# Kernel tuning notes

Measured on AMD Instinct MI355X. Metric: run time of the kernel, lower is better.

## Reference

```python
import jax, jax.numpy as jnp
import numpy as np

RATIO = 0.5          # drop_config[0]; gradually=False so epoch scaling is unused
NUM_BATCHES = 32     # number of distinct batch indices in the sparse coords


def setup_inputs() -> dict:
    key = jax.random.key(0)
    k1, k2, k3 = jax.random.split(key, 3)
    N, C = 1_000_000, 64
    batch_idx = jnp.sort(jax.random.randint(k1, (N,), 0, NUM_BATCHES)).astype(jnp.int32)
    feats = jax.random.normal(k2, (N, C), dtype=jnp.float32)
    scores = jax.random.uniform(k3, (N,), dtype=jnp.float32)  # per-point sampling key
    return {"feats": feats, "batch_idx": batch_idx, "scores": scores}


def _keep_mask(batch_idx, scores):
    """Per batch segment b, drop the floor(n_b * RATIO) points with lowest score
    (equivalent in distribution to np.random.choice without replacement)."""
    N = scores.shape[0]
    counts = jax.ops.segment_sum(jnp.ones((N,), jnp.int32), batch_idx,
                                 num_segments=NUM_BATCHES)              # [B]
    starts = jnp.cumsum(counts) - counts                                 # exclusive prefix [B]
    order = jnp.lexsort((scores, batch_idx))                             # sort by (batch, score)
    pos = jnp.zeros((N,), jnp.int32).at[order].set(
        jnp.arange(N, dtype=jnp.int32))                                  # global sorted position
    rank = pos - starts[batch_idx]                                       # rank within own segment
    n_drop = jnp.floor(counts.astype(jnp.float32) * RATIO).astype(jnp.int32)
    return (rank >= n_drop[batch_idx]).astype(scores.dtype)              # 1 = keep, 0 = dropped


def reference(feats, batch_idx, scores):
    # MinkowskiPruning removes dropped rows; with static shapes we express the
    # identical math as masking features to zero (the module's alternate return path).
    mask = _keep_mask(batch_idx, scores)
    return feats * mask[:, None]
```

## Files before the change

### kernel.cpp

```cpp
#include <hip/hip_runtime.h>
#include <stdint.h>

#define NBATCH 32
#define NSUB   64
#define SUBCAP 128
#define CAPTOT 6144
#define CAP2   512

typedef unsigned long long u64;
typedef unsigned int u32;
typedef float f4 __attribute__((ext_vector_type(4)));

struct WsHdr {
  u64 keysel[NBATCH];
  int counts[NBATCH];
};

__device__ __forceinline__ u32 ordbits(float s) {
  u32 u = __float_as_uint(s);
  return (u & 0x80000000u) ? ~u : (u | 0x80000000u);
}
__device__ __forceinline__ u32 obL() { return ordbits(0.46f); }
__device__ __forceinline__ u32 obR() { return ordbits(0.54f); }


__global__ void k_zero(u32* __restrict__ p, int nwords) {
  int stride = gridDim.x * blockDim.x;
  for (int i = blockIdx.x * blockDim.x + threadIdx.x; i < nwords; i += stride)
    p[i] = 0u;
}

__global__ void k_pass1(const int* __restrict__ batch, const float* __restrict__ scores,
                        int n, u32* __restrict__ meta, u64* __restrict__ cand) {
  __shared__ int h[NBATCH], hl[NBATCH];
  if (threadIdx.x < NBATCH) { h[threadIdx.x] = 0; hl[threadIdx.x] = 0; }
  __syncthreads();
  int sub = blockIdx.x & (NSUB - 1);
  int i = blockIdx.x * blockDim.x + threadIdx.x;
  if (i < n) {
    int b = batch[i];
    u32 ob = ordbits(scores[i]);
    bool lo = ob < obL();
    u64 act = __ballot(1);
    int lead = (int)__ffsll((long long)act) - 1;
    int b0 = __shfl(b, lead, 64);
    bool uni = (__ballot(b == b0) == act);
    if (uni) {
      u64 lom = __ballot(lo);
      if ((threadIdx.x & 63) == lead) {
        atomicAdd(&h[b0], (int)__popcll(act));
        if (lom) atomicAdd(&hl[b0], (int)__popcll(lom));
      }
    } else {
      atomicAdd(&h[b], 1);
      if (lo) atomicAdd(&hl[b], 1);
    }
    if (!lo && ob < obR()) {
      int cell = (b << 6) | sub;
      int p = (int)atomicAdd(&meta[(cell << 4) + 2], 1u);
      if (p < SUBCAP)
        cand[(size_t)cell * SUBCAP + p] = ((u64)ob << 24) | (u32)i;
    }
  }
  __syncthreads();
  if (threadIdx.x < NBATCH) {
    int cell = (threadIdx.x << 6) | sub;
    if (h[threadIdx.x])  atomicAdd(&meta[(cell << 4) + 0], (u32)h[threadIdx.x]);
    if (hl[threadIdx.x]) atomicAdd(&meta[(cell << 4) + 1], (u32)hl[threadIdx.x]);
  }
}

__global__ void k_final(const float* __restrict__ scores, const u32* __restrict__ meta,
                        const u64* __restrict__ cand, WsHdr* ws) {
  __shared__ u64 ck[CAPTOT];
  __shared__ u64 ck2[CAP2];
  __shared__ int sc[256];
  __shared__ int moff[NSUB + 1];
  __shared__ int sh_w, sh_krem, sh_m2, sh_cnt, sh_clo, sh_bad, sh_start;
  int b = blockIdx.x, t = threadIdx.x;

  if (t < NSUB) {
    const u32* mp = meta + (((b << 6) | t) << 4);
    int mc = (int)mp[0], ml = (int)mp[1], mw = (int)mp[2];
    u64 bad = __ballot(mw > SUBCAP);
    int v = mw < SUBCAP ? mw : SUBCAP;
    for (int d = 1; d < 64; d <<= 1) { int u = __shfl_up(v, d, 64); if (t >= d) v += u; }
    moff[t + 1] = v; if (t == 0) moff[0] = 0;
    int s1 = mc, s2 = ml;
    for (int off = 32; off > 0; off >>= 1) {
      s1 += __shfl_down(s1, off, 64);
      s2 += __shfl_down(s2, off, 64);
    }
    if (t == 0) { sh_cnt = s1; sh_clo = s2; sh_bad = (bad != 0ull); }
  }
  __syncthreads();
  int cnt = sh_cnt;
  if (cnt == 0) { if (t == 0) ws->keysel[b] = 0ull; return; }
  int krem = cnt >> 1;
  int m = moff[NSUB];
  int krem2 = krem - sh_clo;
  bool fast = !sh_bad && krem2 >= 0 && krem2 < m && m <= CAPTOT;

  if (fast) {
    const u32 span = obR() - obL();
    for (int sub = 0; sub < NSUB; ++sub) {
      int cw = moff[sub + 1] - moff[sub];
      const u64* src = cand + (size_t)((b << 6) | sub) * SUBCAP;
      for (int j = t; j < cw; j += 256) ck[moff[sub] + j] = src[j];
    }
    sc[t] = 0;
    if (t == 0) sh_m2 = 0;
    __syncthreads();
    for (int j = t; j < m; j += 256) {
      u32 ob = (u32)(ck[j] >> 24);
      u32 bk = (u32)(((u64)(ob - obL()) << 8) / span);
      atomicAdd(&sc[bk], 1);
    }
    __syncthreads();
    int own = sc[t];
    for (int off = 1; off < 256; off <<= 1) {
      int v = (t >= off) ? sc[t - off] : 0;
      __syncthreads(); sc[t] += v; __syncthreads();
    }
    int excl = sc[t] - own;
    if (krem2 >= excl && krem2 < excl + own) { sh_w = t; sh_krem = krem2 - excl; }
    __syncthreads();
    int W = sh_w, krem3 = sh_krem;
    for (int j = t; j < m; j += 256) {
      u32 ob = (u32)(ck[j] >> 24);
      u32 bk = (u32)(((u64)(ob - obL()) << 8) / span);
      if ((int)bk == W) {
        int p = atomicAdd(&sh_m2, 1);
        if (p < CAP2) ck2[p] = ck[j];
      }
    }
    __syncthreads();
    int m2 = sh_m2;
    if (m2 <= CAP2) {
      for (int j = t; j < m2; j += 256) {
        u64 key = ck2[j];
        int r = 0;
        for (int q = 0; q < m2; ++q) r += (ck2[q] < key);
        if (r == krem3) ws->keysel[b] = key;
      }
      return;
    }
    __syncthreads();
  }

  {
    int acc = 0;
    for (int idx = t; idx < b * NSUB; idx += 256)
      acc += (int)meta[((idx / NSUB) == (idx / NSUB) ? (((idx / NSUB) << 6) | (idx & (NSUB - 1))) : 0) << 4];
    sc[t] = acc; __syncthreads();
    for (int off = 128; off > 0; off >>= 1) {
      if (t < off) sc[t] += sc[t + off];
      __syncthreads();
    }
    if (t == 0) sh_start = sc[0];
    __syncthreads();
  }
  int start = sh_start;
  u64 prefix = 0; int kr = krem;
  for (int shift = 48; shift >= 0; shift -= 8) {
    sc[t] = 0;
    __syncthreads();
    for (int idx = t; idx < cnt; idx += 256) {
      u64 key = ((u64)ordbits(scores[start + idx]) << 24) | (u32)(start + idx);
      if ((key >> (shift + 8)) == prefix) atomicAdd(&sc[(int)((key >> shift) & 255)], 1);
    }
    __syncthreads();
    int own = sc[t];
    for (int off = 1; off < 256; off <<= 1) {
      int v = (t >= off) ? sc[t - off] : 0;
      __syncthreads(); sc[t] += v; __syncthreads();
    }
    int excl = sc[t] - own;
    if (kr >= excl && kr < excl + own) { sh_w = t; sh_krem = kr - excl; }
    __syncthreads();
    prefix = (prefix << 8) | (u32)sh_w;
    kr = sh_krem;
    __syncthreads();
  }
  if (t == 0) ws->keysel[b] = prefix;
}

__global__ void k_apply(const f4* __restrict__ feats4,
                        const int* __restrict__ batch,
                        const float* __restrict__ scores,
                        const WsHdr* __restrict__ ws,
                        f4* __restrict__ out4, int n) {
  int t = threadIdx.x;
  int pl = t >> 4, ch = t & 15;
  int i = blockIdx.x * 16 + pl;
  if (i >= n) return;
  int b = batch[i];
  u64 key = ((u64)ordbits(scores[i]) << 24) | (u32)i;
  size_t off = (size_t)i * 16 + (size_t)ch;
  f4 v;
  if (key >= ws->keysel[b]) {
    v = __builtin_nontemporal_load(feats4 + off);
  } else {
    v = (f4){0.f, 0.f, 0.f, 0.f};
  }
  __builtin_nontemporal_store(v, out4 + off);
}


__global__ void k_zero_hdr(WsHdr* ws) {
  int t = threadIdx.x;
  if (t < NBATCH) ws->counts[t] = 0;
}

__global__ void k_hist_fb(const int* __restrict__ batch, int n, WsHdr* ws) {
  __shared__ int h[NBATCH];
  if (threadIdx.x < NBATCH) h[threadIdx.x] = 0;
  __syncthreads();
  int stride = gridDim.x * blockDim.x;
  for (int i = blockIdx.x * blockDim.x + threadIdx.x; i < n; i += stride)
    atomicAdd(&h[batch[i]], 1);
  __syncthreads();
  if (threadIdx.x < NBATCH) atomicAdd(&ws->counts[threadIdx.x], h[threadIdx.x]);
}

__global__ void k_select_fb(const float* __restrict__ scores, WsHdr* ws) {
  __shared__ u32 hist[256];
  __shared__ u64 sh_prefix;
  __shared__ int sh_krem, sh_start;
  int b = blockIdx.x, t = threadIdx.x;
  if (t == 0) {
    int acc = 0; for (int x = 0; x < b; ++x) acc += ws->counts[x];
    sh_start = acc; sh_prefix = 0ull; sh_krem = ws->counts[b] >> 1;
  }
  __syncthreads();
  int start = sh_start, cnt = ws->counts[b];
  if (cnt == 0) { if (t == 0) ws->keysel[b] = 0ull; return; }
  for (int shift = 48; shift >= 0; shift -= 8) {
    for (int j = t; j < 256; j += blockDim.x) hist[j] = 0;
    __syncthreads();
    u64 prefix = sh_prefix;
    for (int idx = t; idx < cnt; idx += blockDim.x) {
      u64 key = ((u64)ordbits(scores[start + idx]) << 24) | (u32)(start + idx);
      if ((key >> (shift + 8)) == prefix)
        atomicAdd(&hist[(u32)(key >> shift) & 255u], 1u);
    }
    __syncthreads();
    if (t == 0) {
      int krem = sh_krem;
      u32 cum = 0, sel = 255;
      for (int j = 0; j < 256; ++j) {
        u32 c = hist[j];
        if ((u32)krem < cum + c) { sel = (u32)j; krem -= (int)cum; break; }
        cum += c;
      }
      sh_prefix = (sh_prefix << 8) | sel;
      sh_krem = krem;
    }
    __syncthreads();
  }
  if (t == 0) ws->keysel[b] = sh_prefix;
}

extern "C" void kernel_launch(void* const* d_in, const int* in_sizes, int n_in,
                              void* d_out, int out_size, void* d_ws, size_t ws_size,
                              hipStream_t stream) {
  const float* feats  = (const float*)d_in[0];
  const int*   batch  = (const int*)d_in[1];
  const float* scores = (const float*)d_in[2];
  float* out = (float*)d_out;
  int n = in_sizes[1];
  WsHdr* ws = (WsHdr*)d_ws;

  const size_t meta_bytes = (size_t)NBATCH * NSUB * 16 * sizeof(u32);
  const size_t cand_bytes = (size_t)NBATCH * NSUB * SUBCAP * sizeof(u64);
  const size_t need = sizeof(WsHdr) + meta_bytes + cand_bytes;

  if (ws_size >= need) {
    u32* meta = (u32*)((char*)d_ws + sizeof(WsHdr));
    u64* cand = (u64*)((char*)d_ws + sizeof(WsHdr) + meta_bytes);
    int nwords = (int)((sizeof(WsHdr) + meta_bytes) / 4);
    int pb = (n + 255) / 256;
    k_zero  <<<128, 256, 0, stream>>>((u32*)d_ws, nwords);
    k_pass1 <<<pb, 256, 0, stream>>>(batch, scores, n, meta, cand);
    k_final <<<NBATCH, 256, 0, stream>>>(scores, meta, cand, ws);
  } else {
    k_zero_hdr <<<1, 64, 0, stream>>>(ws);
    k_hist_fb  <<<1024, 256, 0, stream>>>(batch, n, ws);
    k_select_fb<<<NBATCH, 256, 0, stream>>>(scores, ws);
  }

  int blocks = (n + 15) / 16;
  k_apply<<<blocks, 256, 0, stream>>>((const f4*)feats, batch, scores, ws,
                                      (f4*)out, n);
}
```

Measured before the change: 133.1 us.

## Replace global atomic candidate buckets with per-block compacted candidate lists

Pass 1 now has each block handle 1024 points (4 per thread). Instead of global atomics into per-(batch,sub) cells, each block writes plain per-block histograms and a prefix-sum-compacted candidate list, with the batch id packed into the key's high bits. This removes the zeroing kernel and the global atomic contention. In exchange, the final kernel must scan every block's metadata and candidates and filter by batch, adding serial per-thread loops in the 32 select blocks.

```diff
diff --git a/kernel.cpp b/kernel.cpp
--- a/kernel.cpp
+++ b/kernel.cpp
@@ -2,8 +2,10 @@
 #include <stdint.h>
 
 #define NBATCH 32
-#define NSUB   64
-#define SUBCAP 128
+#define VPT    4
+#define BPTS   1024
+#define CAP_BLK 256
+#define MSTRIDE 72
 #define CAPTOT 6144
 #define CAP2   512
 
@@ -24,93 +26,112 @@
 __device__ __forceinline__ u32 obR() { return ordbits(0.54f); }
 
 
-__global__ void k_zero(u32* __restrict__ p, int nwords) {
-  int stride = gridDim.x * blockDim.x;
-  for (int i = blockIdx.x * blockDim.x + threadIdx.x; i < nwords; i += stride)
-    p[i] = 0u;
-}
-
 __global__ void k_pass1(const int* __restrict__ batch, const float* __restrict__ scores,
                         int n, u32* __restrict__ meta, u64* __restrict__ cand) {
-  __shared__ int h[NBATCH], hl[NBATCH];
-  if (threadIdx.x < NBATCH) { h[threadIdx.x] = 0; hl[threadIdx.x] = 0; }
-  __syncthreads();
-  int sub = blockIdx.x & (NSUB - 1);
-  int i = blockIdx.x * blockDim.x + threadIdx.x;
-  if (i < n) {
-    int b = batch[i];
-    u32 ob = ordbits(scores[i]);
-    bool lo = ob < obL();
-    u64 act = __ballot(1);
-    int lead = (int)__ffsll((long long)act) - 1;
-    int b0 = __shfl(b, lead, 64);
-    bool uni = (__ballot(b == b0) == act);
-    if (uni) {
-      u64 lom = __ballot(lo);
-      if ((threadIdx.x & 63) == lead) {
-        atomicAdd(&h[b0], (int)__popcll(act));
-        if (lom) atomicAdd(&hl[b0], (int)__popcll(lom));
-      }
-    } else {
-      atomicAdd(&h[b], 1);
-      if (lo) atomicAdd(&hl[b], 1);
-    }
-    if (!lo && ob < obR()) {
-      int cell = (b << 6) | sub;
-      int p = (int)atomicAdd(&meta[(cell << 4) + 2], 1u);
-      if (p < SUBCAP)
-        cand[(size_t)cell * SUBCAP + p] = ((u64)ob << 24) | (u32)i;
-    }
-  }
-  __syncthreads();
-  if (threadIdx.x < NBATCH) {
-    int cell = (threadIdx.x << 6) | sub;
-    if (h[threadIdx.x])  atomicAdd(&meta[(cell << 4) + 0], (u32)h[threadIdx.x]);
-    if (hl[threadIdx.x]) atomicAdd(&meta[(cell << 4) + 1], (u32)hl[threadIdx.x]);
-  }
+  __shared__ int hc[NBATCH], hl[NBATCH];
+  __shared__ int sc[256];
+  int t = threadIdx.x, blk = blockIdx.x;
+  if (t < NBATCH) { hc[t] = 0; hl[t] = 0; }
+  __syncthreads();
+
+  u64 wk[VPT]; int wcnt = 0;
+  int i0 = blk * BPTS + t * VPT;
+  #pragma unroll
+  for (int v = 0; v < VPT; ++v) {
+    int i = i0 + v;
+    if (i < n) {
+      int b = batch[i];
+      u32 ob = ordbits(scores[i]);
+      bool lo = ob < obL();
+      u64 act = __ballot(1);
+      int lead = (int)__ffsll((long long)act) - 1;
+      int b0 = __shfl(b, lead, 64);
+      bool uni = (__ballot(b == b0) == act);
+      if (uni) {
+        u64 lom = __ballot(lo);
+        if ((t & 63) == lead) {
+          atomicAdd(&hc[b0], (int)__popcll(act));
+          if (lom) atomicAdd(&hl[b0], (int)__popcll(lom));
+        }
+      } else {
+        atomicAdd(&hc[b], 1);
+        if (lo) atomicAdd(&hl[b], 1);
+      }
+      if (!lo && ob < obR())
+        wk[wcnt++] = ((u64)(u32)b << 56) | ((u64)ob << 24) | (u32)i;
+    }
+  }
+  sc[t] = wcnt; __syncthreads();
+  for (int off = 1; off < 256; off <<= 1) {
+    int v = (t >= off) ? sc[t - off] : 0;
+    __syncthreads(); sc[t] += v; __syncthreads();
+  }
+  int excl = sc[t] - wcnt;
+  int m = sc[255];
+  u64* dst = cand + (size_t)blk * CAP_BLK;
+  for (int j = 0; j < wcnt; ++j)
+    if (excl + j < CAP_BLK) dst[excl + j] = wk[j];
+  __syncthreads();
+  u32* mrow = meta + (size_t)blk * MSTRIDE;
+  if (t < NBATCH) { mrow[t] = (u32)hc[t]; mrow[NBATCH + t] = (u32)hl[t]; }
+  if (t == 0) mrow[64] = (u32)m;
 }
 
 __global__ void k_final(const float* __restrict__ scores, const u32* __restrict__ meta,
-                        const u64* __restrict__ cand, WsHdr* ws) {
+                        int nblk, const u64* __restrict__ cand, WsHdr* ws) {
   __shared__ u64 ck[CAPTOT];
   __shared__ u64 ck2[CAP2];
   __shared__ int sc[256];
-  __shared__ int moff[NSUB + 1];
-  __shared__ int sh_w, sh_krem, sh_m2, sh_cnt, sh_clo, sh_bad, sh_start;
+  __shared__ int sh_w, sh_krem, sh_m, sh_m2, sh_cnt, sh_clo, sh_bad, sh_start;
   int b = blockIdx.x, t = threadIdx.x;
 
-  if (t < NSUB) {
-    const u32* mp = meta + (((b << 6) | t) << 4);
-    int mc = (int)mp[0], ml = (int)mp[1], mw = (int)mp[2];
-    u64 bad = __ballot(mw > SUBCAP);
-    int v = mw < SUBCAP ? mw : SUBCAP;
-    for (int d = 1; d < 64; d <<= 1) { int u = __shfl_up(v, d, 64); if (t >= d) v += u; }
-    moff[t + 1] = v; if (t == 0) moff[0] = 0;
-    int s1 = mc, s2 = ml;
-    for (int off = 32; off > 0; off >>= 1) {
-      s1 += __shfl_down(s1, off, 64);
-      s2 += __shfl_down(s2, off, 64);
-    }
-    if (t == 0) { sh_cnt = s1; sh_clo = s2; sh_bad = (bad != 0ull); }
-  }
-  __syncthreads();
+  {
+    int c = 0, l = 0, bad = 0;
+    for (int blk = t; blk < nblk; blk += 256) {
+      const u32* mrow = meta + (size_t)blk * MSTRIDE;
+      u32 cb = mrow[b];
+      c += (int)cb;
+      l += (int)mrow[NBATCH + b];
+      if (cb && mrow[64] > CAP_BLK) bad = 1;
+    }
+    sc[t] = c; __syncthreads();
+    for (int off = 128; off > 0; off >>= 1) { if (t < off) sc[t] += sc[t + off]; __syncthreads(); }
+    if (t == 0) sh_cnt = sc[0];
+    __syncthreads();
+    sc[t] = l; __syncthreads();
+    for (int off = 128; off > 0; off >>= 1) { if (t < off) sc[t] += sc[t + off]; __syncthreads(); }
+    if (t == 0) sh_clo = sc[0];
+    __syncthreads();
+    sc[t] = bad; __syncthreads();
+    for (int off = 128; off > 0; off >>= 1) { if (t < off) sc[t] |= sc[t + off]; __syncthreads(); }
+    if (t == 0) { sh_bad = sc[0]; sh_m = 0; sh_m2 = 0; }
+    __syncthreads();
+  }
   int cnt = sh_cnt;
   if (cnt == 0) { if (t == 0) ws->keysel[b] = 0ull; return; }
   int krem = cnt >> 1;
-  int m = moff[NSUB];
+
+  for (int blk = t; blk < nblk; blk += 256) {
+    const u32* mrow = meta + (size_t)blk * MSTRIDE;
+    if (mrow[b] == 0) continue;
+    int cc = (int)mrow[64]; if (cc > CAP_BLK) cc = CAP_BLK;
+    const u64* src = cand + (size_t)blk * CAP_BLK;
+    for (int j = 0; j < cc; ++j) {
+      u64 s = src[j];
+      if ((int)(s >> 56) == b) {
+        int p = atomicAdd(&sh_m, 1);
+        if (p < CAPTOT) ck[p] = s;
+      }
+    }
+  }
+  __syncthreads();
+  int m = sh_m;
   int krem2 = krem - sh_clo;
-  bool fast = !sh_bad && krem2 >= 0 && krem2 < m && m <= CAPTOT;
+  bool fast = !sh_bad && m <= CAPTOT && krem2 >= 0 && krem2 < m;
 
   if (fast) {
     const u32 span = obR() - obL();
-    for (int sub = 0; sub < NSUB; ++sub) {
-      int cw = moff[sub + 1] - moff[sub];
-      const u64* src = cand + (size_t)((b << 6) | sub) * SUBCAP;
-      for (int j = t; j < cw; j += 256) ck[moff[sub] + j] = src[j];
-    }
-    sc[t] = 0;
-    if (t == 0) sh_m2 = 0;
-    __syncthreads();
+    sc[t] = 0; __syncthreads();
     for (int j = t; j < m; j += 256) {
       u32 ob = (u32)(ck[j] >> 24);
       u32 bk = (u32)(((u64)(ob - obL()) << 8) / span);
@@ -141,7 +162,7 @@
         u64 key = ck2[j];
         int r = 0;
         for (int q = 0; q < m2; ++q) r += (ck2[q] < key);
-        if (r == krem3) ws->keysel[b] = key;
+        if (r == krem3) ws->keysel[b] = key & 0x00FFFFFFFFFFFFFFull;
       }
       return;
     }
@@ -150,13 +171,12 @@
 
   {
     int acc = 0;
-    for (int idx = t; idx < b * NSUB; idx += 256)
-      acc += (int)meta[((idx / NSUB) == (idx / NSUB) ? (((idx / NSUB) << 6) | (idx & (NSUB - 1))) : 0) << 4];
+    for (int blk = t; blk < nblk; blk += 256) {
+      const u32* mrow = meta + (size_t)blk * MSTRIDE;
+      for (int x = 0; x < b; ++x) acc += (int)mrow[x];
+    }
     sc[t] = acc; __syncthreads();
-    for (int off = 128; off > 0; off >>= 1) {
-      if (t < off) sc[t] += sc[t + off];
-      __syncthreads();
-    }
+    for (int off = 128; off > 0; off >>= 1) { if (t < off) sc[t] += sc[t + off]; __syncthreads(); }
     if (t == 0) sh_start = sc[0];
     __syncthreads();
   }
@@ -271,18 +291,16 @@
   int n = in_sizes[1];
   WsHdr* ws = (WsHdr*)d_ws;
 
-  const size_t meta_bytes = (size_t)NBATCH * NSUB * 16 * sizeof(u32);
-  const size_t cand_bytes = (size_t)NBATCH * NSUB * SUBCAP * sizeof(u64);
+  int nblk = (n + BPTS - 1) / BPTS;
+  const size_t meta_bytes = (size_t)nblk * MSTRIDE * sizeof(u32);
+  const size_t cand_bytes = (size_t)nblk * CAP_BLK * sizeof(u64);
   const size_t need = sizeof(WsHdr) + meta_bytes + cand_bytes;
 
   if (ws_size >= need) {
     u32* meta = (u32*)((char*)d_ws + sizeof(WsHdr));
     u64* cand = (u64*)((char*)d_ws + sizeof(WsHdr) + meta_bytes);
-    int nwords = (int)((sizeof(WsHdr) + meta_bytes) / 4);
-    int pb = (n + 255) / 256;
-    k_zero  <<<128, 256, 0, stream>>>((u32*)d_ws, nwords);
-    k_pass1 <<<pb, 256, 0, stream>>>(batch, scores, n, meta, cand);
-    k_final <<<NBATCH, 256, 0, stream>>>(scores, meta, cand, ws);
+    k_pass1<<<nblk, 256, 0, stream>>>(batch, scores, n, meta, cand);
+    k_final<<<NBATCH, 256, 0, stream>>>(scores, meta, nblk, cand, ws);
   } else {
     k_zero_hdr <<<1, 64, 0, stream>>>(ws);
     k_hist_fb  <<<1024, 256, 0, stream>>>(batch, n, ws);
```

Result: faster. 130.3 us (-2.1%).
